# Optimization experiments

Hardware: AMD Instinct MI355X
Metric: run time of the kernel (lower is better)

The kernel has to match this reference:

```python
import jax, jax.numpy as jnp
import numpy as np

BATCH, D_IN, D_HIDDEN, K = 4096, 2048, 16384, 64


def setup_inputs() -> dict:
    key = jax.random.key(0)
    kx, kw = jax.random.split(key)
    x = jax.random.normal(kx, (BATCH, D_IN), dtype=jnp.float32)
    # W init as in the module: randn normalized per column (dim=0) then scaled by 0.1
    W = jax.random.normal(kw, (D_IN, D_HIDDEN), dtype=jnp.float32)
    W = 0.1 * W / jnp.linalg.norm(W, axis=0, keepdims=True)
    b_enc = jnp.zeros((D_HIDDEN,), dtype=jnp.float32)
    b_dec = jnp.zeros((D_IN,), dtype=jnp.float32)
    return {"x": x, "W": W, "b_enc": b_enc, "b_dec": b_dec, "k": K}


def reference(x, W, b_enc, b_dec, k):
    # encode: linear + ReLU
    f = jax.nn.relu(x @ W + b_enc)            # [B, D_HIDDEN]
    # global batch top-k: keep k * batch largest activations across the whole batch
    flat = f.reshape(-1)                      # [B * D_HIDDEN]
    n_keep = k * x.shape[0]                   # static python int
    vals, idx = jax.lax.top_k(flat, n_keep)
    f_topk = jnp.zeros_like(flat).at[idx].set(vals).reshape(f.shape)
    # tied decode
    recon = f_topk @ W.T + b_dec              # [B, D_IN]
    return (recon, f_topk)
```

## Files before the change

### kernel.cpp

```cpp
#include <hip/hip_runtime.h>
#include <stdint.h>


#define BATCH 4096
#define DIN   2048
#define DHID  16384
#define NELEM (BATCH * DHID)
#define RECON_ELEMS (BATCH * DIN)
#define NBINS 8192
#define THRESH_BIN 1664
#define SC_THRESH 0.203125f
#define WIN   8
#define RLCAP 256
#define CBUF2 512
#define NB2 (NBINS - THRESH_BIN)
#define NB2H (NB2 / 2)
#define SCHUNK 32
#define NCH ((NB2 + SCHUNK - 1) / SCHUNK)
#define NKT 32
#define SBUF8 4096

#define XB_OFF   0u
#define HIST_OFF 16777216u
#define META_OFF (HIST_OFF + 32768u)
#define CAND_OFF (HIST_OFF + 65536u)
#define CANDCAP  80000u
#define SC_OFF   18874368u
#define SCCAP    1835008u

#define M_CNT   0
#define M_BLO   1
#define M_BHI   2
#define M_NNEED 3
#define M_NSURE 4
#define M_OVF   5
#define M_SCCNT 6

struct Cand { unsigned long long key; unsigned int idx; float val; };

typedef short bf16x8 __attribute__((ext_vector_type(8)));
typedef float f32x4  __attribute__((ext_vector_type(4)));

__device__ __forceinline__ int binof(float v) {
    int b = (int)(v * 8192.0f);
    return b > (NBINS - 1) ? (NBINS - 1) : b;
}

__device__ __forceinline__ unsigned short f2bf(float f) {
    unsigned u = __float_as_uint(f);
    unsigned r = 0x7FFFu + ((u >> 16) & 1u);
    return (unsigned short)((u + r) >> 16);
}

__device__ __forceinline__ void gload_lds16(const void* g, void* l) {
    __builtin_amdgcn_global_load_lds(
        (const __attribute__((address_space(1))) void*)g,
        (__attribute__((address_space(3))) void*)l, 16, 0, 0);
}

__device__ __forceinline__ void nt_store4(const float4& v, float* p) {
    f32x4 x = {v.x, v.y, v.z, v.w};
    __builtin_nontemporal_store(x, (f32x4*)p);
}

__global__ void init_kernel(unsigned* __restrict__ hist, unsigned* __restrict__ meta) {
    int i = blockIdx.x * 256 + threadIdx.x;
    if (i < NBINS) hist[i] = 0u;
    if (i < 64)    meta[i] = 0u;
}

__global__ __launch_bounds__(256) void convert_x_init(const float* __restrict__ X,
                                                      unsigned short* __restrict__ Xb,
                                                      unsigned* __restrict__ hist,
                                                      unsigned* __restrict__ meta,
                                                      unsigned* __restrict__ rowcnt) {
    const int bid = blockIdx.x;
    size_t i = (size_t)bid * 256 + threadIdx.x;
    float4 v = ((const float4*)X)[i];
    ushort4 o;
    o.x = f2bf(v.x); o.y = f2bf(v.y); o.z = f2bf(v.z); o.w = f2bf(v.w);
    ((ushort4*)Xb)[i] = o;
    if (bid < 32) {
        int g = bid * 256 + threadIdx.x;
        if (g < NBINS)  hist[g] = 0u;
        if (g < 64)     meta[g] = 0u;
        if (g < BATCH)  rowcnt[g] = 0u;
    }
}

__global__ __launch_bounds__(256) void transpose_both(const float* __restrict__ W,
                                                      float* __restrict__ WT,
                                                      unsigned short* __restrict__ WbT) {
    __shared__ float tile[64][68];
    const int t  = threadIdx.x;
    const int gx = blockIdx.x;
    const int gy = blockIdx.y;
    const int ra = t >> 4;
    const int ca = (t & 15) * 4;
#pragma unroll
    for (int u = 0; u < 4; ++u) {
        int row = u * 16 + ra;
        float4 v = *(const float4*)&W[(size_t)(gy * 64 + row) * DHID + gx * 64 + ca];
        tile[ca + 0][row] = v.x;
        tile[ca + 1][row] = v.y;
        tile[ca + 2][row] = v.z;
        tile[ca + 3][row] = v.w;
    }
    __syncthreads();
#pragma unroll
    for (int u = 0; u < 4; ++u) {
        int cl = u * 16 + ra;
        float4 v = *(const float4*)&tile[cl][ca];
        size_t o = (size_t)(gx * 64 + cl) * DIN + gy * 64 + ca;
        *(float4*)&WT[o] = v;
        ushort4 b;
        b.x = f2bf(v.x); b.y = f2bf(v.y); b.z = f2bf(v.z); b.w = f2bf(v.w);
        *(ushort4*)&WbT[o] = b;
    }
}


#define STAGE_A(H, KT) do { if ((KT) < NKT) {                                   \
    const unsigned short* _s = Xb + (size_t)(m0 + (H)*128 + stgrow)*2048        \
                               + (KT)*64 + stgcol;                              \
    unsigned short* _d = lds + ((H)*2 + ((KT)&1))*8192 + stgdst;                \
    gload_lds16(_s, _d);                                                        \
    gload_lds16(_s + 64*2048, _d + 4096);                                       \
} } while (0)

#define STAGE_B(H, KT) do { if ((KT) < NKT) {                                   \
    const unsigned short* _s = WbT + (size_t)(n0 + (H)*128 + stgrow)*2048       \
                               + (KT)*64 + stgcol;                              \
    unsigned short* _d = lds + 32768 + ((H)*2 + ((KT)&1))*8192 + stgdst;        \
    gload_lds16(_s, _d);                                                        \
    gload_lds16(_s + 64*2048, _d + 4096);                                       \
} } while (0)

#define PHASE(Q, PAR, AH, BH, ...) do {                                         \
    bf16x8 av[4][2], bv[2][2];                                                  \
    _Pragma("unroll")                                                           \
    for (int i = 0; i < 4; ++i) {                                               \
        const unsigned short* _p = lds + ((AH)*2+(PAR))*8192                    \
                                   + (wr2*64 + i*16 + lm)*64;                   \
        av[i][0] = *(const bf16x8*)(_p + cs0);                                  \
        av[i][1] = *(const bf16x8*)(_p + cs1);                                  \
    }                                                                           \
    _Pragma("unroll")                                                           \
    for (int j = 0; j < 2; ++j) {                                               \
        const unsigned short* _p = lds + 32768 + ((BH)*2+(PAR))*8192            \
                                   + (wn*32 + j*16 + lm)*64;                    \
        bv[j][0] = *(const bf16x8*)(_p + cs0);                                  \
        bv[j][1] = *(const bf16x8*)(_p + cs1);                                  \
    }                                                                           \
    __VA_ARGS__                                                                 \
    __builtin_amdgcn_s_barrier();                                               \
    asm volatile("s_waitcnt lgkmcnt(0)" ::: "memory");                          \
    __builtin_amdgcn_sched_barrier(0);                                          \
    __builtin_amdgcn_s_setprio(1);                                              \
    _Pragma("unroll")                                                           \
    for (int i = 0; i < 4; ++i)                                                 \
    _Pragma("unroll")                                                           \
    for (int j = 0; j < 2; ++j) {                                               \
        acc[Q][i][j] = __builtin_amdgcn_mfma_f32_16x16x32_bf16(                 \
            av[i][0], bv[j][0], acc[Q][i][j], 0, 0, 0);                         \
        acc[Q][i][j] = __builtin_amdgcn_mfma_f32_16x16x32_bf16(                 \
            av[i][1], bv[j][1], acc[Q][i][j], 0, 0, 0);                         \
    }                                                                           \
    __builtin_amdgcn_s_setprio(0);                                              \
    __builtin_amdgcn_s_barrier();                                               \
    asm volatile("" ::: "memory");                                              \
} while (0)

__global__ __launch_bounds__(512, 2) void encode_mfma8(const unsigned short* __restrict__ Xb,
                                                       const unsigned short* __restrict__ WbT,
                                                       const float* __restrict__ benc,
                                                       unsigned long long* __restrict__ sc,
                                                       unsigned* __restrict__ meta,
                                                       unsigned* __restrict__ hist,
                                                       float* __restrict__ F) {
    __shared__ unsigned short lds[65536];
    __shared__ unsigned hsh[NB2H];
    __shared__ unsigned s_n, s_base;

    const int t   = threadIdx.x;
    const int wid = t >> 6;
    const int l   = t & 63;
    const int wr2 = wid >> 2;
    const int wn  = wid & 3;
    const int lm  = l & 15;
    const int l7  = l & 7;
    const int cs0 = ((l >> 4) * 8) ^ (l7 * 8);
    const int cs1 = cs0 ^ 32;
    const int stgrow = wid * 8 + (l >> 3);
    const int stgcol = (l7 ^ (l >> 3)) * 8;
    const int stgdst = wid * 512;

    if (t == 0) s_n = 0u;
    for (int i2 = t; i2 < NB2H; i2 += 512) hsh[i2] = 0u;

    const unsigned id  = blockIdx.x;
    const unsigned xcd = id & 7u;
    const unsigned c   = id >> 3;
    const int bx = (int)(xcd * 8u + (c & 7u));
    const int by = (int)(c >> 3);
    const int m0 = by * 256;
    const int n0 = bx * 256;

    f32x4 acc[4][4][2];
#pragma unroll
    for (int q = 0; q < 4; ++q)
#pragma unroll
        for (int i = 0; i < 4; ++i)
#pragma unroll
            for (int j = 0; j < 2; ++j) acc[q][i][j] = (f32x4){0.f, 0.f, 0.f, 0.f};

    STAGE_A(0, 0); STAGE_B(0, 0); STAGE_B(1, 0); STAGE_A(1, 0);
    STAGE_A(0, 1); STAGE_B(1, 1);
    asm volatile("s_waitcnt vmcnt(4)" ::: "memory");
    __builtin_amdgcn_s_barrier();
    asm volatile("" ::: "memory");

#pragma unroll 1
    for (int it = 0; it < 16; ++it) {
        const int T = 2 * it;
        PHASE(0, 0, 0, 0, STAGE_B(0, T + 1); STAGE_A(1, T + 1););
        PHASE(1, 0, 0, 1, (void)0;);
        PHASE(2, 0, 1, 1, STAGE_A(0, T + 2););
        PHASE(3, 0, 1, 0, STAGE_B(1, T + 2);
                          asm volatile("s_waitcnt vmcnt(4)" ::: "memory"););
        PHASE(0, 1, 0, 0, STAGE_B(0, T + 2); STAGE_A(1, T + 2););
        PHASE(1, 1, 0, 1, (void)0;);
        PHASE(2, 1, 1, 1, STAGE_A(0, T + 3););
        PHASE(3, 1, 1, 0, STAGE_B(1, T + 3);
                          asm volatile("s_waitcnt vmcnt(4)" ::: "memory"););
    }

    __syncthreads();
    unsigned long long* sbuf = (unsigned long long*)lds;

#pragma unroll
    for (int q = 0; q < 4; ++q) {
        const int qm = (q >= 2) ? 1 : 0;
        const int qn = (q == 1 || q == 2) ? 1 : 0;
#pragma unroll
        for (int j = 0; j < 2; ++j) {
            const int col = n0 + qn * 128 + wn * 32 + j * 16 + lm;
            const float bias = benc[col];
#pragma unroll
            for (int i = 0; i < 4; ++i) {
                const int rbase = m0 + qm * 128 + wr2 * 64 + i * 16 + (l >> 4) * 4;
#pragma unroll
                for (int r = 0; r < 4; ++r) {
                    float v = fmaxf(acc[q][i][j][r] + bias, 0.0f);
                    if (v >= SC_THRESH) {
                        unsigned hx = (unsigned)(binof(v) - THRESH_BIN);
                        atomicAdd(&hsh[hx >> 1], (hx & 1u) ? 65536u : 1u);
                        unsigned flat = (unsigned)(rbase + r) * (unsigned)DHID + (unsigned)col;
                        unsigned long long e =
                            ((unsigned long long)__float_as_uint(v) << 32) | flat;
                        unsigned pos = atomicAdd(&s_n, 1u);
                        if (pos < SBUF8) sbuf[pos] = e;
                        else {
                            unsigned p = atomicAdd(&meta[M_SCCNT], 1u);
                            if (p < SCCAP) sc[p] = e; else meta[M_OVF] = 1u;
                        }
                    }
                }
            }
        }
    }
    {
        const float4 z4 = {0.f, 0.f, 0.f, 0.f};
        const int zr = t >> 6;
        const int zc = (t & 63) * 4;
#pragma unroll 1
        for (int rr = 0; rr < 32; ++rr)
            nt_store4(z4, &F[(size_t)(m0 + zr + rr * 8) * DHID + n0 + zc]);
    }
    __syncthreads();
    unsigned n = s_n < SBUF8 ? s_n : (unsigned)SBUF8;
    if (t == 0) s_base = atomicAdd(&meta[M_SCCNT], n);
    __syncthreads();
    const unsigned base = s_base;
    for (unsigned l2 = t; l2 < n; l2 += 512) {
        unsigned p = base + l2;
        if (p < SCCAP) sc[p] = sbuf[l2]; else meta[M_OVF] = 1u;
    }
    for (int i2 = t; i2 < NB2H; i2 += 512) {
        unsigned u = hsh[i2];
        unsigned lo = u & 0xFFFFu, hi = u >> 16;
        if (lo) atomicAdd(&hist[THRESH_BIN + 2 * i2], lo);
        if (hi) atomicAdd(&hist[THRESH_BIN + 2 * i2 + 1], hi);
    }
}

__global__ void scan_sc(const unsigned* __restrict__ hist,
                        unsigned* __restrict__ meta,
                        const int* __restrict__ kptr) {
    __shared__ unsigned sh[NB2];
    __shared__ unsigned csum[NCH];
    int t = threadIdx.x;
    for (int i = t; i < NB2; i += 256) sh[i] = hist[THRESH_BIN + i];
    __syncthreads();
    if (t < NCH) {
        unsigned s = 0;
        int base = t * SCHUNK;
        for (int u = 0; u < SCHUNK && base + u < NB2; ++u) s += sh[base + u];
        csum[t] = s;
    }
    __syncthreads();
    if (t == 0) {
        unsigned nk = (unsigned)kptr[0] * BATCH;
        unsigned cum = 0;
        int bstar_idx = -1;
        for (int c = NCH - 1; c >= 0; --c) {
            if (cum + csum[c] >= nk) {
                int hi2 = c * SCHUNK + SCHUNK - 1; if (hi2 >= NB2) hi2 = NB2 - 1;
                for (int idx = hi2; idx >= c * SCHUNK; --idx) {
                    cum += sh[idx];
                    if (cum >= nk) { bstar_idx = idx; break; }
                }
                break;
            } else cum += csum[c];
        }
        if (bstar_idx < 0) { meta[M_OVF] = 2u; bstar_idx = WIN; }
        int bstar = THRESH_BIN + bstar_idx;
        int blo = bstar - WIN;
        if (blo < THRESH_BIN) { meta[M_OVF] = 3u; blo = THRESH_BIN; }
        int bhi = bstar + WIN; if (bhi > NBINS - 1) bhi = NBINS - 1;
        int bhi_idx = bhi - THRESH_BIN;
        unsigned nsure = 0;
        int cstart = (bhi_idx + 1 + SCHUNK - 1) / SCHUNK;
        for (int idx = bhi_idx + 1; idx < cstart * SCHUNK && idx < NB2; ++idx) nsure += sh[idx];
        for (int c = cstart; c < NCH; ++c) nsure += csum[c];
        meta[M_BLO]   = (unsigned)blo;
        meta[M_BHI]   = (unsigned)bhi;
        meta[M_NSURE] = nsure;
        meta[M_NNEED] = nk - nsure;
    }
}

__global__ __launch_bounds__(256) void emit_sc(const unsigned long long* __restrict__ sc,
                                               unsigned* __restrict__ meta,
                                               Cand* __restrict__ cand,
                                               unsigned* __restrict__ rowcnt,
                                               unsigned long long* __restrict__ rowlist) {
    __shared__ uint2 s_cand[CBUF2];
    __shared__ unsigned s_nc, s_base;
    const int tid = threadIdx.x;
    if (tid == 0) s_nc = 0u;
    __syncthreads();
    const unsigned blo = meta[M_BLO], bhi = meta[M_BHI];
    unsigned C = meta[M_SCCNT]; if (C > SCCAP) C = SCCAP;
    size_t stride = (size_t)gridDim.x * 256;
    for (size_t i = (size_t)blockIdx.x * 256 + tid; i < C; i += stride) {
        unsigned long long e = sc[i];
        unsigned vbits = (unsigned)(e >> 32);
        unsigned idx   = (unsigned)(e & 0xFFFFFFFFu);
        unsigned b = (unsigned)binof(__uint_as_float(vbits));
        if (b > bhi) {
            unsigned row = idx >> 14;
            unsigned pos = atomicAdd(&rowcnt[row], 1u);
            if (pos < RLCAP)
                rowlist[(size_t)row * RLCAP + pos] =
                    ((unsigned long long)vbits << 32) | (idx & (DHID - 1));
            else meta[M_OVF] = 1u;
        } else if (b >= blo) {
            unsigned pos = atomicAdd(&s_nc, 1u);
            if (pos < CBUF2) { s_cand[pos].x = idx; s_cand[pos].y = vbits; }
            else {
                unsigned p = atomicAdd(&meta[M_CNT], 1u);
                if (p < CANDCAP) { cand[p].idx = idx; cand[p].val = __uint_as_float(vbits); }
                else meta[M_OVF] = 1u;
            }
        }
    }
    __syncthreads();
    unsigned nc = s_nc < CBUF2 ? s_nc : (unsigned)CBUF2;
    if (tid == 0) s_base = atomicAdd(&meta[M_CNT], nc);
    __syncthreads();
    const unsigned base = s_base;
    for (unsigned l2 = tid; l2 < nc; l2 += 256) {
        unsigned p = base + l2;
        if (p < CANDCAP) { cand[p].idx = s_cand[l2].x; cand[p].val = __uint_as_float(s_cand[l2].y); }
        else meta[M_OVF] = 1u;
    }
}

__global__ __launch_bounds__(64) void scatter_rl(const unsigned long long* __restrict__ rowlist,
                                                 const unsigned* __restrict__ rowcnt,
                                                 float* __restrict__ F) {
    int b = blockIdx.x;
    unsigned cnt = rowcnt[b]; if (cnt > RLCAP) cnt = RLCAP;
    for (unsigned l = threadIdx.x; l < cnt; l += 64) {
        unsigned long long e = rowlist[(size_t)b * RLCAP + l];
        unsigned j = (unsigned)(e & 0xFFFFFFFFu);
        F[(size_t)b * DHID + j] = __uint_as_float((unsigned)(e >> 32));
    }
}

__global__ __launch_bounds__(256) void exact_wave(const float* __restrict__ X,
                                                  const float* __restrict__ WT,
                                                  const float* __restrict__ benc,
                                                  const unsigned* __restrict__ meta,
                                                  Cand* __restrict__ cand) {
    unsigned C = meta[M_CNT]; if (C > CANDCAP) C = CANDCAP;
    const int lane = threadIdx.x & 63;
    const unsigned wid = blockIdx.x * 4 + (threadIdx.x >> 6);
    const unsigned nw  = gridDim.x * 4;
    for (unsigned c = wid; c < C; c += nw) {
        unsigned idx = cand[c].idx;
        int b = (int)(idx >> 14);
        int j = (int)(idx & (DHID - 1));
        const float4* x4 = (const float4*)(X  + (size_t)b * DIN);
        const float4* w4 = (const float4*)(WT + (size_t)j * DIN);
        double acc = 0.0;
#pragma unroll
        for (int u = 0; u < 8; ++u) {
            float4 xv = x4[lane + 64 * u];
            float4 wv = w4[lane + 64 * u];
            acc += (double)xv.x * (double)wv.x + (double)xv.y * (double)wv.y
                 + (double)xv.z * (double)wv.z + (double)xv.w * (double)wv.w;
        }
#pragma unroll
        for (int off = 32; off > 0; off >>= 1)
            acc += __shfl_down(acc, off, 64);
        if (lane == 0) {
            double v = acc + (double)benc[j];
            if (v < 0.0) v = 0.0;
            cand[c].key = (unsigned long long)__double_as_longlong(v);
        }
    }
}

__global__ __launch_bounds__(1024) void select_kernel(unsigned* __restrict__ meta,
                                                      Cand* __restrict__ cand) {
    __shared__ unsigned h[4096];
    __shared__ unsigned csum[128];
    __shared__ unsigned long long s_prefix;
    __shared__ unsigned s_need, s_gcnt;
    __shared__ unsigned long long gkey[1024];
    __shared__ unsigned gpos[1024];
    __shared__ unsigned gidx[1024];
    __shared__ unsigned char gkeep[1024];

    int t = threadIdx.x;
    unsigned C = meta[M_CNT]; if (C > CANDCAP) C = CANDCAP;
    if (t == 0) { s_prefix = 0ULL; s_need = meta[M_NNEED]; s_gcnt = 0u; }
    __syncthreads();

    for (int pass = 0; pass < 3; ++pass) {
        for (int i = t; i < 4096; i += 1024) h[i] = 0u;
        __syncthreads();
        int shift = 52 - pass * 12;
        unsigned long long pfx = s_prefix;
        for (unsigned c = t; c < C; c += 1024) {
            unsigned long long key = cand[c].key;
            if (pass == 0 || (key >> (shift + 12)) == pfx)
                atomicAdd(&h[(unsigned)((key >> shift) & 0xFFFULL)], 1u);
        }
        __syncthreads();
        if (t < 128) {
            unsigned s = 0;
#pragma unroll
            for (int u = 0; u < 32; ++u) s += h[t * 32 + u];
            csum[t] = s;
        }
        __syncthreads();
        if (t == 0) {
            unsigned need = s_need;
            unsigned cum2 = 0; int cc = 127;
            for (; cc >= 0; --cc) {
                if (cum2 + csum[cc] >= need) break;
                cum2 += csum[cc];
            }
            int bsel = 0;
            if (cc >= 0) {
                unsigned cum3 = cum2;
                for (int b = cc * 32 + 31; b >= cc * 32; --b) {
                    cum3 += h[b];
                    if (cum3 >= need) { bsel = b; s_need = need - (cum3 - h[b]); break; }
                }
            }
            s_prefix = (s_prefix << 12) | (unsigned long long)bsel;
        }
        __syncthreads();
    }
    unsigned long long pfx = s_prefix;
    for (unsigned c = t; c < C; c += 1024) {
        unsigned long long key = cand[c].key;
        if ((key >> 28) == pfx) {
            unsigned p = atomicAdd(&s_gcnt, 1u);
            if (p < 1024) { gkey[p] = key; gpos[p] = c; gidx[p] = cand[c].idx; gkeep[p] = 0; }
        }
    }
    __syncthreads();
    if (t == 0) {
        unsigned g = s_gcnt < 1024u ? s_gcnt : 1024u;
        unsigned nd = s_need;
        for (unsigned sel = 0; sel < nd && sel < g; ++sel) {
            int best = -1;
            for (unsigned i = 0; i < g; ++i) {
                if (gkeep[i]) continue;
                if (best < 0 || gkey[i] > gkey[best] ||
                    (gkey[i] == gkey[best] && gidx[i] < gidx[best])) best = (int)i;
            }
            if (best >= 0) gkeep[best] = 1;
        }
        for (unsigned i = 0; i < g; ++i)
            if (gkeep[i]) cand[gpos[i]].idx = gidx[i] | 0x80000000u;
    }
    __syncthreads();
    for (unsigned c = t; c < C; c += 1024)
        if ((cand[c].key >> 28) > pfx) cand[c].idx |= 0x80000000u;
}

__global__ __launch_bounds__(256) void restore2_kernel(float* __restrict__ F,
                                                       const unsigned* __restrict__ meta,
                                                       const Cand* __restrict__ cand,
                                                       unsigned* __restrict__ rowcnt,
                                                       unsigned long long* __restrict__ rowlist) {
    unsigned C = meta[M_CNT]; if (C > CANDCAP) C = CANDCAP;
    size_t stride = (size_t)gridDim.x * 256;
    for (size_t c = (size_t)blockIdx.x * 256 + threadIdx.x; c < C; c += stride) {
        unsigned id = cand[c].idx;
        if (id & 0x80000000u) {
            unsigned idx = id & 0x7FFFFFFFu;
            float v = (float)__longlong_as_double((long long)cand[c].key);
            F[idx] = v;
            unsigned row = idx >> 14;
            unsigned j   = idx & (DHID - 1);
            unsigned pos = atomicAdd(&rowcnt[row], 1u);
            if (pos < RLCAP)
                rowlist[(size_t)row * RLCAP + pos] =
                    ((unsigned long long)__float_as_uint(v) << 32) | j;
        }
    }
}

__global__ __launch_bounds__(256) void decode_rl_f32(const unsigned long long* __restrict__ rowlist,
                                                     const unsigned* __restrict__ rowcnt,
                                                     const float* __restrict__ WT,
                                                     const float* __restrict__ bdec,
                                                     float* __restrict__ recon) {
    __shared__ unsigned sj[RLCAP];
    __shared__ float    sv[RLCAP];
    int b = blockIdx.x;
    int t = threadIdx.x;
    unsigned cnt = rowcnt[b]; if (cnt > RLCAP) cnt = RLCAP;
    for (unsigned l = t; l < cnt; l += 256) {
        unsigned long long e = rowlist[(size_t)b * RLCAP + l];
        sj[l] = (unsigned)(e & 0xFFFFFFFFu);
        sv[l] = __uint_as_float((unsigned)(e >> 32));
    }
    __syncthreads();
    float4 acc0 = {0, 0, 0, 0}, acc1 = {0, 0, 0, 0};
    for (unsigned l = 0; l < cnt; ++l) {
        float v = sv[l]; unsigned j = sj[l];
        const float4* w4 = (const float4*)(WT + (size_t)j * DIN);
        float4 wa = w4[t], wb = w4[256 + t];
        acc0.x = fmaf(v, wa.x, acc0.x); acc0.y = fmaf(v, wa.y, acc0.y);
        acc0.z = fmaf(v, wa.z, acc0.z); acc0.w = fmaf(v, wa.w, acc0.w);
        acc1.x = fmaf(v, wb.x, acc1.x); acc1.y = fmaf(v, wb.y, acc1.y);
        acc1.z = fmaf(v, wb.z, acc1.z); acc1.w = fmaf(v, wb.w, acc1.w);
    }
    float4 bd0 = ((const float4*)bdec)[t];
    float4 bd1 = ((const float4*)bdec)[256 + t];
    float4 o0 = {acc0.x + bd0.x, acc0.y + bd0.y, acc0.z + bd0.z, acc0.w + bd0.w};
    float4 o1 = {acc1.x + bd1.x, acc1.y + bd1.y, acc1.z + bd1.z, acc1.w + bd1.w};
    float* dst = recon + (size_t)b * DIN;
    nt_store4(o0, dst + 4 * t);
    nt_store4(o1, dst + 4 * (256 + t));
}

__global__ __launch_bounds__(256) void decode_rl_bf16(const unsigned long long* __restrict__ rowlist,
                                                      const unsigned* __restrict__ rowcnt,
                                                      const unsigned short* __restrict__ WbT,
                                                      const float* __restrict__ bdec,
                                                      float* __restrict__ recon) {
    __shared__ unsigned sj[RLCAP];
    __shared__ float    sv[RLCAP];
    int b = blockIdx.x;
    int t = threadIdx.x;
    unsigned cnt = rowcnt[b]; if (cnt > RLCAP) cnt = RLCAP;
    for (unsigned l = t; l < cnt; l += 256) {
        unsigned long long e = rowlist[(size_t)b * RLCAP + l];
        sj[l] = (unsigned)(e & 0xFFFFFFFFu);
        sv[l] = __uint_as_float((unsigned)(e >> 32));
    }
    __syncthreads();
    float4 acc0 = {0, 0, 0, 0}, acc1 = {0, 0, 0, 0};
    unsigned l = 0;
    for (; l + 2 <= cnt; l += 2) {
        float v0 = sv[l], v1 = sv[l + 1];
        const ushort4* w0 = (const ushort4*)(WbT + (size_t)sj[l]     * DIN);
        const ushort4* w1 = (const ushort4*)(WbT + (size_t)sj[l + 1] * DIN);
        ushort4 a0 = w0[t], b0 = w0[256 + t];
        ushort4 a1 = w1[t], b1 = w1[256 + t];
        acc0.x = fmaf(v0, __uint_as_float((unsigned)a0.x << 16), acc0.x);
        acc0.y = fmaf(v0, __uint_as_float((unsigned)a0.y << 16), acc0.y);
        acc0.z = fmaf(v0, __uint_as_float((unsigned)a0.z << 16), acc0.z);
        acc0.w = fmaf(v0, __uint_as_float((unsigned)a0.w << 16), acc0.w);
        acc1.x = fmaf(v0, __uint_as_float((unsigned)b0.x << 16), acc1.x);
        acc1.y = fmaf(v0, __uint_as_float((unsigned)b0.y << 16), acc1.y);
        acc1.z = fmaf(v0, __uint_as_float((unsigned)b0.z << 16), acc1.z);
        acc1.w = fmaf(v0, __uint_as_float((unsigned)b0.w << 16), acc1.w);
        acc0.x = fmaf(v1, __uint_as_float((unsigned)a1.x << 16), acc0.x);
        acc0.y = fmaf(v1, __uint_as_float((unsigned)a1.y << 16), acc0.y);
        acc0.z = fmaf(v1, __uint_as_float((unsigned)a1.z << 16), acc0.z);
        acc0.w = fmaf(v1, __uint_as_float((unsigned)a1.w << 16), acc0.w);
        acc1.x = fmaf(v1, __uint_as_float((unsigned)b1.x << 16), acc1.x);
        acc1.y = fmaf(v1, __uint_as_float((unsigned)b1.y << 16), acc1.y);
        acc1.z = fmaf(v1, __uint_as_float((unsigned)b1.z << 16), acc1.z);
        acc1.w = fmaf(v1, __uint_as_float((unsigned)b1.w << 16), acc1.w);
    }
    if (l < cnt) {
        float v0 = sv[l];
        const ushort4* w0 = (const ushort4*)(WbT + (size_t)sj[l] * DIN);
        ushort4 a0 = w0[t], b0 = w0[256 + t];
        acc0.x = fmaf(v0, __uint_as_float((unsigned)a0.x << 16), acc0.x);
        acc0.y = fmaf(v0, __uint_as_float((unsigned)a0.y << 16), acc0.y);
        acc0.z = fmaf(v0, __uint_as_float((unsigned)a0.z << 16), acc0.z);
        acc0.w = fmaf(v0, __uint_as_float((unsigned)a0.w << 16), acc0.w);
        acc1.x = fmaf(v0, __uint_as_float((unsigned)b0.x << 16), acc1.x);
        acc1.y = fmaf(v0, __uint_as_float((unsigned)b0.y << 16), acc1.y);
        acc1.z = fmaf(v0, __uint_as_float((unsigned)b0.z << 16), acc1.z);
        acc1.w = fmaf(v0, __uint_as_float((unsigned)b0.w << 16), acc1.w);
    }
    float4 bd0 = ((const float4*)bdec)[t];
    float4 bd1 = ((const float4*)bdec)[256 + t];
    float4 o0 = {acc0.x + bd0.x, acc0.y + bd0.y, acc0.z + bd0.z, acc0.w + bd0.w};
    float4 o1 = {acc1.x + bd1.x, acc1.y + bd1.y, acc1.z + bd1.z, acc1.w + bd1.w};
    float* dst = recon + (size_t)b * DIN;
    nt_store4(o0, dst + 4 * t);
    nt_store4(o1, dst + 4 * (256 + t));
}

__global__ __launch_bounds__(256) void encode_f32(const float* __restrict__ X,
                                                  const float* __restrict__ W,
                                                  const float* __restrict__ benc,
                                                  float* __restrict__ F) {
    __shared__ float As[16][128];
    __shared__ float Bs[16][128];
    const int t  = threadIdx.x;
    const int n0 = blockIdx.x * 128;
    const int m0 = blockIdx.y * 128;
    const int tx = t & 15, ty = t >> 4;
    const int ra = t >> 1, ca = (t & 1) * 8;
    const int rb = t >> 4, cb = (t & 15) * 8;
    float acc[8][8];
#pragma unroll
    for (int i = 0; i < 8; ++i)
#pragma unroll
        for (int j = 0; j < 8; ++j) acc[i][j] = 0.0f;
    const float* xp = X + (size_t)(m0 + ra) * DIN + ca;
    const float* wp = W + (size_t)rb * DHID + n0 + cb;
    for (int k0 = 0; k0 < DIN; k0 += 16) {
        float4 a0 = *(const float4*)(xp + k0);
        float4 a1 = *(const float4*)(xp + k0 + 4);
        float4 b0 = *(const float4*)(wp + (size_t)k0 * DHID);
        float4 b1 = *(const float4*)(wp + (size_t)k0 * DHID + 4);
        __syncthreads();
        As[ca + 0][ra] = a0.x; As[ca + 1][ra] = a0.y; As[ca + 2][ra] = a0.z; As[ca + 3][ra] = a0.w;
        As[ca + 4][ra] = a1.x; As[ca + 5][ra] = a1.y; As[ca + 6][ra] = a1.z; As[ca + 7][ra] = a1.w;
        *(float4*)&Bs[rb][cb]     = b0;
        *(float4*)&Bs[rb][cb + 4] = b1;
        __syncthreads();
#pragma unroll
        for (int kk = 0; kk < 16; ++kk) {
            float a[8], bb[8];
            *(float4*)&a[0]  = *(const float4*)&As[kk][ty * 8];
            *(float4*)&a[4]  = *(const float4*)&As[kk][ty * 8 + 4];
            *(float4*)&bb[0] = *(const float4*)&Bs[kk][tx * 8];
            *(float4*)&bb[4] = *(const float4*)&Bs[kk][tx * 8 + 4];
#pragma unroll
            for (int i = 0; i < 8; ++i)
#pragma unroll
                for (int j = 0; j < 8; ++j)
                    acc[i][j] = fmaf(a[i], bb[j], acc[i][j]);
        }
    }
    float bias[8];
    *(float4*)&bias[0] = *(const float4*)&benc[n0 + tx * 8];
    *(float4*)&bias[4] = *(const float4*)&benc[n0 + tx * 8 + 4];
#pragma unroll
    for (int i = 0; i < 8; ++i) {
        float out[8];
#pragma unroll
        for (int j = 0; j < 8; ++j) out[j] = fmaxf(acc[i][j] + bias[j], 0.0f);
        float* dst = F + (size_t)(m0 + ty * 8 + i) * DHID + n0 + tx * 8;
        *(float4*)dst       = *(float4*)&out[0];
        *(float4*)(dst + 4) = *(float4*)&out[4];
    }
}

__global__ __launch_bounds__(256) void survey_kernel(const float* __restrict__ F,
                                                     unsigned* __restrict__ hist) {
    __shared__ unsigned h[NBINS];
    for (int i = THRESH_BIN + threadIdx.x; i < NBINS; i += 256) h[i] = 0u;
    __syncthreads();
    const float4* F4 = (const float4*)F;
    size_t stride = (size_t)gridDim.x * 256;
    for (size_t i = (size_t)blockIdx.x * 256 + threadIdx.x; i < NELEM / 4; i += stride) {
        float4 v = F4[i];
        float vv[4] = {v.x, v.y, v.z, v.w};
#pragma unroll
        for (int c = 0; c < 4; ++c) {
            int b = binof(vv[c]);
            if (b >= THRESH_BIN) atomicAdd(&h[b], 1u);
        }
    }
    __syncthreads();
    for (int i2 = THRESH_BIN + threadIdx.x; i2 < NBINS; i2 += 256)
        if (h[i2]) atomicAdd(&hist[i2], h[i2]);
}

__global__ __launch_bounds__(256) void collect_old(const float* __restrict__ F,
                                                   unsigned* __restrict__ meta,
                                                   Cand* __restrict__ cand, unsigned cap) {
    unsigned blo = meta[M_BLO], bhi = meta[M_BHI];
    const float4* F4 = (const float4*)F;
    size_t stride = (size_t)gridDim.x * 256;
    for (size_t i = (size_t)blockIdx.x * 256 + threadIdx.x; i < NELEM / 4; i += stride) {
        float4 v = F4[i];
        float vv[4] = {v.x, v.y, v.z, v.w};
#pragma unroll
        for (int c = 0; c < 4; ++c) {
            unsigned b = (unsigned)binof(vv[c]);
            if (b >= blo && b <= bhi) {
                unsigned p = atomicAdd(&meta[M_CNT], 1u);
                if (p < cap) { cand[p].idx = (unsigned)(i * 4 + c); cand[p].val = vv[c]; }
                else meta[M_OVF] = 1u;
            }
        }
    }
}

__global__ __launch_bounds__(256) void zero_old(float* __restrict__ F,
                                                const unsigned* __restrict__ meta) {
    unsigned bhi = meta[M_BHI];
    float4* F4 = (float4*)F;
    size_t stride = (size_t)gridDim.x * 256;
    for (size_t i = (size_t)blockIdx.x * 256 + threadIdx.x; i < NELEM / 4; i += stride) {
        float4 v = F4[i];
        v.x = ((unsigned)binof(v.x) > bhi) ? v.x : 0.0f;
        v.y = ((unsigned)binof(v.y) > bhi) ? v.y : 0.0f;
        v.z = ((unsigned)binof(v.z) > bhi) ? v.z : 0.0f;
        v.w = ((unsigned)binof(v.w) > bhi) ? v.w : 0.0f;
        F4[i] = v;
    }
}

__global__ __launch_bounds__(256) void exact_old(const float* __restrict__ X,
                                                 const float* __restrict__ W,
                                                 const float* __restrict__ benc,
                                                 const unsigned* __restrict__ meta,
                                                 Cand* __restrict__ cand, unsigned cap) {
    __shared__ double red[256];
    unsigned C = meta[M_CNT]; if (C > cap) C = cap;
    int t = threadIdx.x;
    for (unsigned c = blockIdx.x; c < C; c += gridDim.x) {
        unsigned idx = cand[c].idx;
        int b = (int)(idx >> 14);
        int j = (int)(idx & (DHID - 1));
        const float* xp = X + (size_t)b * DIN + t * 8;
        const float* wp = W + (size_t)(t * 8) * DHID + j;
        double part = 0.0;
#pragma unroll
        for (int u = 0; u < 8; ++u)
            part += (double)xp[u] * (double)wp[(size_t)u * DHID];
        red[t] = part;
        __syncthreads();
        for (int s = 128; s > 0; s >>= 1) {
            if (t < s) red[t] += red[t + s];
            __syncthreads();
        }
        if (t == 0) {
            double v = red[0] + (double)benc[j];
            if (v < 0.0) v = 0.0;
            cand[c].key = (unsigned long long)__double_as_longlong(v);
        }
        __syncthreads();
    }
}

__global__ __launch_bounds__(256) void restore_old(float* __restrict__ F,
                                                   const unsigned* __restrict__ meta,
                                                   const Cand* __restrict__ cand, unsigned cap) {
    unsigned C = meta[M_CNT]; if (C > cap) C = cap;
    size_t stride = (size_t)gridDim.x * 256;
    for (size_t c = (size_t)blockIdx.x * 256 + threadIdx.x; c < C; c += stride) {
        unsigned id = cand[c].idx;
        if (id & 0x80000000u)
            F[id & 0x7FFFFFFFu] = (float)__longlong_as_double((long long)cand[c].key);
    }
}

__global__ __launch_bounds__(256) void decode_old(const float* __restrict__ F,
                                                  const float* __restrict__ W,
                                                  const float* __restrict__ bdec,
                                                  float* __restrict__ recon) {
    __shared__ unsigned sj[4096];
    __shared__ float    sv[4096];
    __shared__ unsigned soff[257];
    int b = blockIdx.x;
    int t = threadIdx.x;
    float4 acc0 = {0, 0, 0, 0}, acc1 = {0, 0, 0, 0};
    const float* frow = F + (size_t)b * DHID;
    for (int seg = 0; seg < 4; ++seg) {
        int base = seg * 4096;
        unsigned cnt = 0;
#pragma unroll
        for (int c = 0; c < 16; ++c)
            if (frow[base + t * 16 + c] != 0.0f) cnt++;
        soff[t] = cnt;
        __syncthreads();
        if (t == 0) {
            unsigned o = 0;
            for (int i = 0; i < 256; ++i) { unsigned tmp = soff[i]; soff[i] = o; o += tmp; }
            soff[256] = o;
        }
        __syncthreads();
        unsigned pos = soff[t];
        for (int c = 0; c < 16; ++c) {
            float v = frow[base + t * 16 + c];
            if (v != 0.0f) { sj[pos] = (unsigned)(base + t * 16 + c); sv[pos] = v; ++pos; }
        }
        __syncthreads();
        unsigned total = soff[256];
        int i0 = t * 4, i1 = 1024 + t * 4;
        for (unsigned l = 0; l < total; ++l) {
            float v = sv[l]; unsigned j = sj[l];
            const float* wp = W + j;
            acc0.x = fmaf(v, wp[(size_t)(i0 + 0) * DHID], acc0.x);
            acc0.y = fmaf(v, wp[(size_t)(i0 + 1) * DHID], acc0.y);
            acc0.z = fmaf(v, wp[(size_t)(i0 + 2) * DHID], acc0.z);
            acc0.w = fmaf(v, wp[(size_t)(i0 + 3) * DHID], acc0.w);
            acc1.x = fmaf(v, wp[(size_t)(i1 + 0) * DHID], acc1.x);
            acc1.y = fmaf(v, wp[(size_t)(i1 + 1) * DHID], acc1.y);
            acc1.z = fmaf(v, wp[(size_t)(i1 + 2) * DHID], acc1.z);
            acc1.w = fmaf(v, wp[(size_t)(i1 + 3) * DHID], acc1.w);
        }
        __syncthreads();
    }
    float4 bd0 = ((const float4*)bdec)[t];
    float4 bd1 = ((const float4*)bdec)[256 + t];
    float4 o0 = {acc0.x + bd0.x, acc0.y + bd0.y, acc0.z + bd0.z, acc0.w + bd0.w};
    float4 o1 = {acc1.x + bd1.x, acc1.y + bd1.y, acc1.z + bd1.z, acc1.w + bd1.w};
    float4* dst = (float4*)(recon + (size_t)b * DIN);
    dst[t]       = o0;
    dst[256 + t] = o1;
}

extern "C" void kernel_launch(void* const* d_in, const int* in_sizes, int n_in,
                              void* d_out, int out_size, void* d_ws, size_t ws_size,
                              hipStream_t stream) {
    const float* X    = (const float*)d_in[0];
    const float* W    = (const float*)d_in[1];
    const float* benc = (const float*)d_in[2];
    const float* bdec = (const float*)d_in[3];
    const int*   kptr = (const int*)d_in[4];

    float* recon = (float*)d_out;
    float* F     = recon + RECON_ELEMS;

    const size_t WT_BYTES  = (size_t)DIN * DHID * sizeof(float);
    const size_t WBT_BYTES = (size_t)DIN * DHID * sizeof(short);
    const size_t ROW_BYTES = 65536 + (size_t)BATCH * RLCAP * 8;
    float* WT = (float*)d_ws;

    if (ws_size >= WT_BYTES + WBT_BYTES) {
        unsigned short* WbT = (unsigned short*)((char*)d_ws + WT_BYTES);
        int bf16_decode = (ws_size >= WT_BYTES + WBT_BYTES + ROW_BYTES) ? 1 : 0;
        char* rowbase = bf16_decode ? ((char*)d_ws + WT_BYTES + WBT_BYTES)
                                    : ((char*)WbT);
        unsigned* rowcnt = (unsigned*)rowbase;
        unsigned long long* rowlist = (unsigned long long*)(rowbase + 65536);

        unsigned short* Xb = (unsigned short*)((char*)d_out + XB_OFF);
        unsigned* hist = (unsigned*)((char*)d_out + HIST_OFF);
        unsigned* meta = (unsigned*)((char*)d_out + META_OFF);
        Cand*     cand = (Cand*)((char*)d_out + CAND_OFF);
        unsigned long long* sc = (unsigned long long*)((char*)d_out + SC_OFF);

        convert_x_init<<<dim3(8192), dim3(256), 0, stream>>>(X, Xb, hist, meta, rowcnt);
        transpose_both<<<dim3(256, 32), dim3(256), 0, stream>>>(W, WT, WbT);
        encode_mfma8<<<dim3(1024), dim3(512), 0, stream>>>(Xb, WbT, benc, sc, meta, hist, F);
        scan_sc<<<dim3(1), dim3(256), 0, stream>>>(hist, meta, kptr);
        emit_sc<<<dim3(512), dim3(256), 0, stream>>>(sc, meta, cand, rowcnt, rowlist);
        scatter_rl<<<dim3(4096), dim3(64), 0, stream>>>(rowlist, rowcnt, F);
        exact_wave<<<dim3(4096), dim3(256), 0, stream>>>(X, WT, benc, meta, cand);
        select_kernel<<<dim3(1), dim3(1024), 0, stream>>>(meta, cand);
        restore2_kernel<<<dim3(1024), dim3(256), 0, stream>>>(F, meta, cand, rowcnt, rowlist);
        if (bf16_decode)
            decode_rl_bf16<<<dim3(4096), dim3(256), 0, stream>>>(rowlist, rowcnt, WbT, bdec, recon);
        else
            decode_rl_f32<<<dim3(4096), dim3(256), 0, stream>>>(rowlist, rowcnt, WT, bdec, recon);
    } else {
        unsigned* hist = (unsigned*)d_out;
        unsigned* meta = hist + NBINS;
        Cand*     cand = (Cand*)((char*)d_out + 65536);
        const unsigned cap = 1000000u;

        init_kernel<<<dim3(33), dim3(256), 0, stream>>>(hist, meta);
        encode_f32<<<dim3(128, 32), dim3(256), 0, stream>>>(X, W, benc, F);
        survey_kernel<<<dim3(2048), dim3(256), 0, stream>>>(F, hist);
        scan_sc<<<dim3(1), dim3(256), 0, stream>>>(hist, meta, kptr);
        collect_old<<<dim3(2048), dim3(256), 0, stream>>>(F, meta, cand, cap);
        exact_old<<<dim3(4096), dim3(256), 0, stream>>>(X, W, benc, meta, cand, cap);
        select_kernel<<<dim3(1), dim3(1024), 0, stream>>>(meta, cand);
        zero_old<<<dim3(2048), dim3(256), 0, stream>>>(F, meta);
        restore_old<<<dim3(1024), dim3(256), 0, stream>>>(F, meta, cand, cap);
        decode_old<<<dim3(4096), dim3(256), 0, stream>>>(F, W, bdec, recon);
    }
}
```

Baseline: 747.1 us.

## Switch encode GEMM to scaled fp16 MFMA and narrow exact-rescore window

Converts X and the transposed W to fp16 (W pre-scaled by 256 to stay in range) and uses f16 MFMA instead of bf16, undoing the scale in the epilogue and in the decode. The higher mantissa precision lets the refinement window WIN shrink from 8 to 3 bins, so fewer candidates need exact fp64 rescoring. The exact rescoring kernel also processes two candidates per wave to raise memory-level parallelism. Risks include fp16 overflow or underflow and misselection near the top-k threshold if the narrower window misses true candidates.

Measured after the change: 722.5 us. 3.3% less time.

```diff
diff --git a/kernel.cpp b/kernel.cpp
--- a/kernel.cpp
+++ b/kernel.cpp
@@ -10,7 +10,7 @@
 #define NBINS 8192
 #define THRESH_BIN 1664
 #define SC_THRESH 0.203125f
-#define WIN   8
+#define WIN   3
 #define RLCAP 256
 #define CBUF2 512
 #define NB2 (NBINS - THRESH_BIN)
@@ -19,6 +19,7 @@
 #define NCH ((NB2 + SCHUNK - 1) / SCHUNK)
 #define NKT 32
 #define SBUF8 4096
+#define WSCALE_INV 0.00390625f
 
 #define XB_OFF   0u
 #define HIST_OFF 16777216u
@@ -38,7 +39,7 @@
 
 struct Cand { unsigned long long key; unsigned int idx; float val; };
 
-typedef short bf16x8 __attribute__((ext_vector_type(8)));
+typedef _Float16 f16x8 __attribute__((ext_vector_type(8)));
 typedef float f32x4  __attribute__((ext_vector_type(4)));
 
 __device__ __forceinline__ int binof(float v) {
@@ -46,10 +47,13 @@
     return b > (NBINS - 1) ? (NBINS - 1) : b;
 }
 
-__device__ __forceinline__ unsigned short f2bf(float f) {
-    unsigned u = __float_as_uint(f);
-    unsigned r = 0x7FFFu + ((u >> 16) & 1u);
-    return (unsigned short)((u + r) >> 16);
+__device__ __forceinline__ unsigned short f2h(float f) {
+    _Float16 h = (_Float16)f;
+    return __builtin_bit_cast(unsigned short, h);
+}
+
+__device__ __forceinline__ float h2f(unsigned short u) {
+    return (float)__builtin_bit_cast(_Float16, u);
 }
 
 __device__ __forceinline__ void gload_lds16(const void* g, void* l) {
@@ -70,7 +74,7 @@
 }
 
 __global__ __launch_bounds__(256) void convert_x_init(const float* __restrict__ X,
-                                                      unsigned short* __restrict__ Xb,
+                                                      unsigned short* __restrict__ Xh,
                                                       unsigned* __restrict__ hist,
                                                       unsigned* __restrict__ meta,
                                                       unsigned* __restrict__ rowcnt) {
@@ -78,8 +82,8 @@
     size_t i = (size_t)bid * 256 + threadIdx.x;
     float4 v = ((const float4*)X)[i];
     ushort4 o;
-    o.x = f2bf(v.x); o.y = f2bf(v.y); o.z = f2bf(v.z); o.w = f2bf(v.w);
-    ((ushort4*)Xb)[i] = o;
+    o.x = f2h(v.x); o.y = f2h(v.y); o.z = f2h(v.z); o.w = f2h(v.w);
+    ((ushort4*)Xh)[i] = o;
     if (bid < 32) {
         int g = bid * 256 + threadIdx.x;
         if (g < NBINS)  hist[g] = 0u;
@@ -90,7 +94,7 @@
 
 __global__ __launch_bounds__(256) void transpose_both(const float* __restrict__ W,
                                                       float* __restrict__ WT,
-                                                      unsigned short* __restrict__ WbT) {
+                                                      unsigned short* __restrict__ WhT) {
     __shared__ float tile[64][68];
     const int t  = threadIdx.x;
     const int gx = blockIdx.x;
@@ -114,14 +118,15 @@
         size_t o = (size_t)(gx * 64 + cl) * DIN + gy * 64 + ca;
         *(float4*)&WT[o] = v;
         ushort4 b;
-        b.x = f2bf(v.x); b.y = f2bf(v.y); b.z = f2bf(v.z); b.w = f2bf(v.w);
-        *(ushort4*)&WbT[o] = b;
+        b.x = f2h(v.x * 256.0f); b.y = f2h(v.y * 256.0f);
+        b.z = f2h(v.z * 256.0f); b.w = f2h(v.w * 256.0f);
+        *(ushort4*)&WhT[o] = b;
     }
 }
 
 
 #define STAGE_A(H, KT) do { if ((KT) < NKT) {                                   \
-    const unsigned short* _s = Xb + (size_t)(m0 + (H)*128 + stgrow)*2048        \
+    const unsigned short* _s = Xh + (size_t)(m0 + (H)*128 + stgrow)*2048        \
                                + (KT)*64 + stgcol;                              \
     unsigned short* _d = lds + ((H)*2 + ((KT)&1))*8192 + stgdst;                \
     gload_lds16(_s, _d);                                                        \
@@ -129,7 +134,7 @@
 } } while (0)
 
 #define STAGE_B(H, KT) do { if ((KT) < NKT) {                                   \
-    const unsigned short* _s = WbT + (size_t)(n0 + (H)*128 + stgrow)*2048       \
+    const unsigned short* _s = WhT + (size_t)(n0 + (H)*128 + stgrow)*2048       \
                                + (KT)*64 + stgcol;                              \
     unsigned short* _d = lds + 32768 + ((H)*2 + ((KT)&1))*8192 + stgdst;        \
     gload_lds16(_s, _d);                                                        \
@@ -137,20 +142,20 @@
 } } while (0)
 
 #define PHASE(Q, PAR, AH, BH, ...) do {                                         \
-    bf16x8 av[4][2], bv[2][2];                                                  \
+    f16x8 av[4][2], bv[2][2];                                                   \
     _Pragma("unroll")                                                           \
     for (int i = 0; i < 4; ++i) {                                               \
         const unsigned short* _p = lds + ((AH)*2+(PAR))*8192                    \
                                    + (wr2*64 + i*16 + lm)*64;                   \
-        av[i][0] = *(const bf16x8*)(_p + cs0);                                  \
-        av[i][1] = *(const bf16x8*)(_p + cs1);                                  \
+        av[i][0] = *(const f16x8*)(_p + cs0);                                   \
+        av[i][1] = *(const f16x8*)(_p + cs1);                                   \
     }                                                                           \
     _Pragma("unroll")                                                           \
     for (int j = 0; j < 2; ++j) {                                               \
         const unsigned short* _p = lds + 32768 + ((BH)*2+(PAR))*8192            \
                                    + (wn*32 + j*16 + lm)*64;                    \
-        bv[j][0] = *(const bf16x8*)(_p + cs0);                                  \
-        bv[j][1] = *(const bf16x8*)(_p + cs1);                                  \
+        bv[j][0] = *(const f16x8*)(_p + cs0);                                   \
+        bv[j][1] = *(const f16x8*)(_p + cs1);                                   \
     }                                                                           \
     __VA_ARGS__                                                                 \
     __builtin_amdgcn_s_barrier();                                               \
@@ -161,9 +166,9 @@
     for (int i = 0; i < 4; ++i)                                                 \
     _Pragma("unroll")                                                           \
     for (int j = 0; j < 2; ++j) {                                               \
-        acc[Q][i][j] = __builtin_amdgcn_mfma_f32_16x16x32_bf16(                 \
+        acc[Q][i][j] = __builtin_amdgcn_mfma_f32_16x16x32_f16(                  \
             av[i][0], bv[j][0], acc[Q][i][j], 0, 0, 0);                         \
-        acc[Q][i][j] = __builtin_amdgcn_mfma_f32_16x16x32_bf16(                 \
+        acc[Q][i][j] = __builtin_amdgcn_mfma_f32_16x16x32_f16(                  \
             av[i][1], bv[j][1], acc[Q][i][j], 0, 0, 0);                         \
     }                                                                           \
     __builtin_amdgcn_s_setprio(0);                                              \
@@ -171,8 +176,8 @@
     asm volatile("" ::: "memory");                                              \
 } while (0)
 
-__global__ __launch_bounds__(512, 2) void encode_mfma8(const unsigned short* __restrict__ Xb,
-                                                       const unsigned short* __restrict__ WbT,
+__global__ __launch_bounds__(512, 2) void encode_mfma8(const unsigned short* __restrict__ Xh,
+                                                       const unsigned short* __restrict__ WhT,
                                                        const float* __restrict__ benc,
                                                        unsigned long long* __restrict__ sc,
                                                        unsigned* __restrict__ meta,
@@ -251,7 +256,7 @@
                 const int rbase = m0 + qm * 128 + wr2 * 64 + i * 16 + (l >> 4) * 4;
 #pragma unroll
                 for (int r = 0; r < 4; ++r) {
-                    float v = fmaxf(acc[q][i][j][r] + bias, 0.0f);
+                    float v = fmaxf(acc[q][i][j][r] * WSCALE_INV + bias, 0.0f);
                     if (v >= SC_THRESH) {
                         unsigned hx = (unsigned)(binof(v) - THRESH_BIN);
                         atomicAdd(&hsh[hx >> 1], (hx & 1u) ? 65536u : 1u);
@@ -408,27 +413,41 @@
     const int lane = threadIdx.x & 63;
     const unsigned wid = blockIdx.x * 4 + (threadIdx.x >> 6);
     const unsigned nw  = gridDim.x * 4;
-    for (unsigned c = wid; c < C; c += nw) {
-        unsigned idx = cand[c].idx;
-        int b = (int)(idx >> 14);
-        int j = (int)(idx & (DHID - 1));
-        const float4* x4 = (const float4*)(X  + (size_t)b * DIN);
-        const float4* w4 = (const float4*)(WT + (size_t)j * DIN);
-        double acc = 0.0;
+    for (unsigned c = wid * 2; c < C; c += nw * 2) {
+        unsigned c1 = c + 1;
+        bool has1 = (c1 < C);
+        unsigned idxA = cand[c].idx;
+        unsigned idxB = cand[has1 ? c1 : c].idx;
+        const float4* xA = (const float4*)(X  + (size_t)(idxA >> 14) * DIN);
+        const float4* wA = (const float4*)(WT + (size_t)(idxA & (DHID - 1)) * DIN);
+        const float4* xB = (const float4*)(X  + (size_t)(idxB >> 14) * DIN);
+        const float4* wB = (const float4*)(WT + (size_t)(idxB & (DHID - 1)) * DIN);
+        double a0 = 0.0, a1 = 0.0;
 #pragma unroll
         for (int u = 0; u < 8; ++u) {
-            float4 xv = x4[lane + 64 * u];
-            float4 wv = w4[lane + 64 * u];
-            acc += (double)xv.x * (double)wv.x + (double)xv.y * (double)wv.y
-                 + (double)xv.z * (double)wv.z + (double)xv.w * (double)wv.w;
-        }
-#pragma unroll
-        for (int off = 32; off > 0; off >>= 1)
-            acc += __shfl_down(acc, off, 64);
+            float4 xa = xA[lane + 64 * u];
+            float4 wa = wA[lane + 64 * u];
+            float4 xb = xB[lane + 64 * u];
+            float4 wb = wB[lane + 64 * u];
+            a0 += (double)xa.x * (double)wa.x + (double)xa.y * (double)wa.y
+                + (double)xa.z * (double)wa.z + (double)xa.w * (double)wa.w;
+            a1 += (double)xb.x * (double)wb.x + (double)xb.y * (double)wb.y
+                + (double)xb.z * (double)wb.z + (double)xb.w * (double)wb.w;
+        }
+#pragma unroll
+        for (int off = 32; off > 0; off >>= 1) {
+            a0 += __shfl_down(a0, off, 64);
+            a1 += __shfl_down(a1, off, 64);
+        }
         if (lane == 0) {
-            double v = acc + (double)benc[j];
-            if (v < 0.0) v = 0.0;
-            cand[c].key = (unsigned long long)__double_as_longlong(v);
+            double v0 = a0 + (double)benc[idxA & (DHID - 1)];
+            if (v0 < 0.0) v0 = 0.0;
+            cand[c].key = (unsigned long long)__double_as_longlong(v0);
+            if (has1) {
+                double v1 = a1 + (double)benc[idxB & (DHID - 1)];
+                if (v1 < 0.0) v1 = 0.0;
+                cand[c1].key = (unsigned long long)__double_as_longlong(v1);
+            }
         }
     }
 }
@@ -573,11 +592,11 @@
     nt_store4(o1, dst + 4 * (256 + t));
 }
 
-__global__ __launch_bounds__(256) void decode_rl_bf16(const unsigned long long* __restrict__ rowlist,
-                                                      const unsigned* __restrict__ rowcnt,
-                                                      const unsigned short* __restrict__ WbT,
-                                                      const float* __restrict__ bdec,
-                                                      float* __restrict__ recon) {
+__global__ __launch_bounds__(256) void decode_rl_f16(const unsigned long long* __restrict__ rowlist,
+                                                     const unsigned* __restrict__ rowcnt,
+                                                     const unsigned short* __restrict__ WhT,
+                                                     const float* __restrict__ bdec,
+                                                     float* __restrict__ recon) {
     __shared__ unsigned sj[RLCAP];
     __shared__ float    sv[RLCAP];
     int b = blockIdx.x;
@@ -586,46 +605,34 @@
     for (unsigned l = t; l < cnt; l += 256) {
         unsigned long long e = rowlist[(size_t)b * RLCAP + l];
         sj[l] = (unsigned)(e & 0xFFFFFFFFu);
-        sv[l] = __uint_as_float((unsigned)(e >> 32));
+        sv[l] = __uint_as_float((unsigned)(e >> 32)) * WSCALE_INV;
     }
     __syncthreads();
     float4 acc0 = {0, 0, 0, 0}, acc1 = {0, 0, 0, 0};
     unsigned l = 0;
     for (; l + 2 <= cnt; l += 2) {
         float v0 = sv[l], v1 = sv[l + 1];
-        const ushort4* w0 = (const ushort4*)(WbT + (size_t)sj[l]     * DIN);
-        const ushort4* w1 = (const ushort4*)(WbT + (size_t)sj[l + 1] * DIN);
+        const ushort4* w0 = (const ushort4*)(WhT + (size_t)sj[l]     * DIN);
+        const ushort4* w1 = (const ushort4*)(WhT + (size_t)sj[l + 1] * DIN);
         ushort4 a0 = w0[t], b0 = w0[256 + t];
         ushort4 a1 = w1[t], b1 = w1[256 + t];
-        acc0.x = fmaf(v0, __uint_as_float((unsigned)a0.x << 16), acc0.x);
-        acc0.y = fmaf(v0, __uint_as_float((unsigned)a0.y << 16), acc0.y);
-        acc0.z = fmaf(v0, __uint_as_float((unsigned)a0.z << 16), acc0.z);
-        acc0.w = fmaf(v0, __uint_as_float((unsigned)a0.w << 16), acc0.w);
-        acc1.x = fmaf(v0, __uint_as_float((unsigned)b0.x << 16), acc1.x);
-        acc1.y = fmaf(v0, __uint_as_float((unsigned)b0.y << 16), acc1.y);
-        acc1.z = fmaf(v0, __uint_as_float((unsigned)b0.z << 16), acc1.z);
-        acc1.w = fmaf(v0, __uint_as_float((unsigned)b0.w << 16), acc1.w);
-        acc0.x = fmaf(v1, __uint_as_float((unsigned)a1.x << 16), acc0.x);
-        acc0.y = fmaf(v1, __uint_as_float((unsigned)a1.y << 16), acc0.y);
-        acc0.z = fmaf(v1, __uint_as_float((unsigned)a1.z << 16), acc0.z);
-        acc0.w = fmaf(v1, __uint_as_float((unsigned)a1.w << 16), acc0.w);
-        acc1.x = fmaf(v1, __uint_as_float((unsigned)b1.x << 16), acc1.x);
-        acc1.y = fmaf(v1, __uint_as_float((unsigned)b1.y << 16), acc1.y);
-        acc1.z = fmaf(v1, __uint_as_float((unsigned)b1.z << 16), acc1.z);
-        acc1.w = fmaf(v1, __uint_as_float((unsigned)b1.w << 16), acc1.w);
+        acc0.x = fmaf(v0, h2f(a0.x), acc0.x); acc0.y = fmaf(v0, h2f(a0.y), acc0.y);
+        acc0.z = fmaf(v0, h2f(a0.z), acc0.z); acc0.w = fmaf(v0, h2f(a0.w), acc0.w);
+        acc1.x = fmaf(v0, h2f(b0.x), acc1.x); acc1.y = fmaf(v0, h2f(b0.y), acc1.y);
+        acc1.z = fmaf(v0, h2f(b0.z), acc1.z); acc1.w = fmaf(v0, h2f(b0.w), acc1.w);
+        acc0.x = fmaf(v1, h2f(a1.x), acc0.x); acc0.y = fmaf(v1, h2f(a1.y), acc0.y);
+        acc0.z = fmaf(v1, h2f(a1.z), acc0.z); acc0.w = fmaf(v1, h2f(a1.w), acc0.w);
+        acc1.x = fmaf(v1, h2f(b1.x), acc1.x); acc1.y = fmaf(v1, h2f(b1.y), acc1.y);
+        acc1.z = fmaf(v1, h2f(b1.z), acc1.z); acc1.w = fmaf(v1, h2f(b1.w), acc1.w);
     }
     if (l < cnt) {
         float v0 = sv[l];
-        const ushort4* w0 = (const ushort4*)(WbT + (size_t)sj[l] * DIN);
+        const ushort4* w0 = (const ushort4*)(WhT + (size_t)sj[l] * DIN);
         ushort4 a0 = w0[t], b0 = w0[256 + t];
-        acc0.x = fmaf(v0, __uint_as_float((unsigned)a0.x << 16), acc0.x);
-        acc0.y = fmaf(v0, __uint_as_float((unsigned)a0.y << 16), acc0.y);
-        acc0.z = fmaf(v0, __uint_as_float((unsigned)a0.z << 16), acc0.z);
-        acc0.w = fmaf(v0, __uint_as_float((unsigned)a0.w << 16), acc0.w);
-        acc1.x = fmaf(v0, __uint_as_float((unsigned)b0.x << 16), acc1.x);
-        acc1.y = fmaf(v0, __uint_as_float((unsigned)b0.y << 16), acc1.y);
-        acc1.z = fmaf(v0, __uint_as_float((unsigned)b0.z << 16), acc1.z);
-        acc1.w = fmaf(v0, __uint_as_float((unsigned)b0.w << 16), acc1.w);
+        acc0.x = fmaf(v0, h2f(a0.x), acc0.x); acc0.y = fmaf(v0, h2f(a0.y), acc0.y);
+        acc0.z = fmaf(v0, h2f(a0.z), acc0.z); acc0.w = fmaf(v0, h2f(a0.w), acc0.w);
+        acc1.x = fmaf(v0, h2f(b0.x), acc1.x); acc1.y = fmaf(v0, h2f(b0.y), acc1.y);
+        acc1.z = fmaf(v0, h2f(b0.z), acc1.z); acc1.w = fmaf(v0, h2f(b0.w), acc1.w);
     }
     float4 bd0 = ((const float4*)bdec)[t];
     float4 bd1 = ((const float4*)bdec)[256 + t];
@@ -865,35 +872,35 @@
     float* F     = recon + RECON_ELEMS;
 
     const size_t WT_BYTES  = (size_t)DIN * DHID * sizeof(float);
-    const size_t WBT_BYTES = (size_t)DIN * DHID * sizeof(short);
+    const size_t WHT_BYTES = (size_t)DIN * DHID * sizeof(short);
     const size_t ROW_BYTES = 65536 + (size_t)BATCH * RLCAP * 8;
     float* WT = (float*)d_ws;
 
-    if (ws_size >= WT_BYTES + WBT_BYTES) {
-        unsigned short* WbT = (unsigned short*)((char*)d_ws + WT_BYTES);
-        int bf16_decode = (ws_size >= WT_BYTES + WBT_BYTES + ROW_BYTES) ? 1 : 0;
-        char* rowbase = bf16_decode ? ((char*)d_ws + WT_BYTES + WBT_BYTES)
-                                    : ((char*)WbT);
+    if (ws_size >= WT_BYTES + WHT_BYTES) {
+        unsigned short* WhT = (unsigned short*)((char*)d_ws + WT_BYTES);
+        int f16_decode = (ws_size >= WT_BYTES + WHT_BYTES + ROW_BYTES) ? 1 : 0;
+        char* rowbase = f16_decode ? ((char*)d_ws + WT_BYTES + WHT_BYTES)
+                                   : ((char*)WhT);
         unsigned* rowcnt = (unsigned*)rowbase;
         unsigned long long* rowlist = (unsigned long long*)(rowbase + 65536);
 
-        unsigned short* Xb = (unsigned short*)((char*)d_out + XB_OFF);
+        unsigned short* Xh = (unsigned short*)((char*)d_out + XB_OFF);
         unsigned* hist = (unsigned*)((char*)d_out + HIST_OFF);
         unsigned* meta = (unsigned*)((char*)d_out + META_OFF);
         Cand*     cand = (Cand*)((char*)d_out + CAND_OFF);
         unsigned long long* sc = (unsigned long long*)((char*)d_out + SC_OFF);
 
-        convert_x_init<<<dim3(8192), dim3(256), 0, stream>>>(X, Xb, hist, meta, rowcnt);
-        transpose_both<<<dim3(256, 32), dim3(256), 0, stream>>>(W, WT, WbT);
-        encode_mfma8<<<dim3(1024), dim3(512), 0, stream>>>(Xb, WbT, benc, sc, meta, hist, F);
+        convert_x_init<<<dim3(8192), dim3(256), 0, stream>>>(X, Xh, hist, meta, rowcnt);
+        transpose_both<<<dim3(256, 32), dim3(256), 0, stream>>>(W, WT, WhT);
+        encode_mfma8<<<dim3(1024), dim3(512), 0, stream>>>(Xh, WhT, benc, sc, meta, hist, F);
         scan_sc<<<dim3(1), dim3(256), 0, stream>>>(hist, meta, kptr);
         emit_sc<<<dim3(512), dim3(256), 0, stream>>>(sc, meta, cand, rowcnt, rowlist);
         scatter_rl<<<dim3(4096), dim3(64), 0, stream>>>(rowlist, rowcnt, F);
         exact_wave<<<dim3(4096), dim3(256), 0, stream>>>(X, WT, benc, meta, cand);
         select_kernel<<<dim3(1), dim3(1024), 0, stream>>>(meta, cand);
         restore2_kernel<<<dim3(1024), dim3(256), 0, stream>>>(F, meta, cand, rowcnt, rowlist);
-        if (bf16_decode)
-            decode_rl_bf16<<<dim3(4096), dim3(256), 0, stream>>>(rowlist, rowcnt, WbT, bdec, recon);
+        if (f16_decode)
+            decode_rl_f16<<<dim3(4096), dim3(256), 0, stream>>>(rowlist, rowcnt, WhT, bdec, recon);
         else
             decode_rl_f32<<<dim3(4096), dim3(256), 0, stream>>>(rowlist, rowcnt, WT, bdec, recon);
     } else {
```
